# Optimization experiments

Measured on AMD Instinct MI355X. Metric: run time of the kernel, lower is better.

## Reference

```python
import jax, jax.numpy as jnp
import numpy as np

N_NODES = 50000
N_EDGES = 1600000
NEG_SLOPE = 0.2


def _gat_layer(x, src, dst, W, a_src, a_dst, b, n_nodes):
    # PyG GATConv (heads=1, concat=True): h = xW; e_ij = LeakyReLU(a_src.h_j + a_dst.h_i)
    # alpha = softmax over incoming edges of each target i; out_i = sum_j alpha_ij h_j + b
    h = x @ W                                   # [N, out]
    alpha_src = h @ a_src                        # [N]
    alpha_dst = h @ a_dst                        # [N]
    e = alpha_src[src] + alpha_dst[dst]          # [E]
    e = jnp.where(e > 0, e, NEG_SLOPE * e)       # leaky_relu(0.2)
    m = jax.ops.segment_max(e, dst, num_segments=n_nodes)   # per-target max
    ex = jnp.exp(e - m[dst])
    denom = jax.ops.segment_sum(ex, dst, num_segments=n_nodes)
    alpha = ex / (denom[dst] + 1e-16)            # [E]
    out = jax.ops.segment_sum(alpha[:, None] * h[src], dst, num_segments=n_nodes)
    return out + b


def setup_inputs() -> dict:
    key = jax.random.key(0)
    ks = jax.random.split(key, 16)
    hid, out_dim, in_dim = 128, 5, 13
    x = jax.random.normal(ks[0], (N_NODES, in_dim), dtype=jnp.float32)
    edge_index = jax.random.randint(ks[1], (2, N_EDGES), 0, N_NODES, dtype=jnp.int64)
    s = 0.1
    return {
        "x": x,
        "edge_index": edge_index,
        "W1": jax.random.normal(ks[2], (in_dim, hid), dtype=jnp.float32) * s,
        "a_src1": jax.random.normal(ks[3], (hid,), dtype=jnp.float32) * s,
        "a_dst1": jax.random.normal(ks[4], (hid,), dtype=jnp.float32) * s,
        "b1": jnp.zeros((hid,), dtype=jnp.float32),
        "W2": jax.random.normal(ks[5], (hid, hid), dtype=jnp.float32) * s,
        "a_src2": jax.random.normal(ks[6], (hid,), dtype=jnp.float32) * s,
        "a_dst2": jax.random.normal(ks[7], (hid,), dtype=jnp.float32) * s,
        "b2": jnp.zeros((hid,), dtype=jnp.float32),
        "W3": jax.random.normal(ks[8], (hid, out_dim), dtype=jnp.float32) * s,
        "a_src3": jax.random.normal(ks[9], (out_dim,), dtype=jnp.float32) * s,
        "a_dst3": jax.random.normal(ks[10], (out_dim,), dtype=jnp.float32) * s,
        "b3": jnp.zeros((out_dim,), dtype=jnp.float32),
    }


def reference(x, edge_index, W1, a_src1, a_dst1, b1, W2, a_src2, a_dst2, b2,
              W3, a_src3, a_dst3, b3):
    n = x.shape[0]
    # GATConv add_self_loops=True: append (i, i) edges
    loops = jnp.arange(n, dtype=edge_index.dtype)
    src = jnp.concatenate([edge_index[0], loops])
    dst = jnp.concatenate([edge_index[1], loops])
    h = _gat_layer(x, src, dst, W1, a_src1, a_dst1, b1, n)
    h = jax.nn.relu(h)  # dropout identity in eval mode
    h = _gat_layer(h, src, dst, W2, a_src2, a_dst2, b2, n)
    h = jax.nn.relu(h)
    h = _gat_layer(h, src, dst, W3, a_src3, a_dst3, b3, n)
    return jax.nn.log_softmax(h, axis=1)
```

## Files before the change

### kernel.cpp

```cpp
#include <hip/hip_runtime.h>
#include <hip/hip_bf16.h>


#define LEAKY(e) ((e) > 0.f ? (e) : 0.2f * (e))
__device__ inline float clamp30(float e) { return fminf(fmaxf(e, -30.f), 30.f); }
__device__ inline float expc(float e) { return __expf(clamp30(LEAKY(e))); }

__device__ inline float ldany(const void* p, int bf, int i) {
    return bf ? __bfloat162float(((const __hip_bfloat16*)p)[i])
              : ((const float*)p)[i];
}
__device__ inline int ldidx(const void* p, int i64, long long i) {
    return i64 ? (int)(((const unsigned int*)p)[2 * i])
               : ((const int*)p)[i];
}

__device__ inline float bflo(unsigned int w) { return __uint_as_float(w << 16); }
__device__ inline float bfhi(unsigned int w) { return __uint_as_float(w & 0xffff0000u); }
__device__ inline unsigned short bfbits(float a) {
    __hip_bfloat16 x = __float2bfloat16(a);
    unsigned short u; __builtin_memcpy(&u, &x, 2); return u;
}
__device__ inline unsigned int packbf(float a, float b) {
    return (unsigned int)bfbits(a) | ((unsigned int)bfbits(b) << 16);
}

typedef __attribute__((ext_vector_type(8))) short short8;
typedef __attribute__((ext_vector_type(4))) float f32x4;

__global__ void detect_kernel(const void* W1, const void* ei, int* flags) {
    if (threadIdx.x == 0 && blockIdx.x == 0) {
        const unsigned int* w = (const unsigned int*)W1;
        int c = 0;
        for (int i = 0; i < 64; i++) {
            unsigned int e = (w[i] >> 7) & 0xFFu;
            if (e >= 0x70u && e <= 0x7Fu) c++;
        }
        flags[0] = (c >= 32) ? 1 : 0;
        const unsigned int* q = (const unsigned int*)ei;
        int z = 0;
        for (int i = 0; i < 64; i++)
            if (q[2 * i + 1] == 0u) z++;
        flags[1] = (z >= 32) ? 1 : 0;
    }
}


__global__ __launch_bounds__(256) void sortA_hist(
    const void* __restrict__ ei, const int* __restrict__ flags,
    int* __restrict__ blockHist, int E, int NBUK)
{
    __shared__ int hist[512];
    const int i64 = flags[1];
    const int tid = threadIdx.x, blk = blockIdx.x;
    for (int i = tid; i < NBUK; i += 256) hist[i] = 0;
    __syncthreads();
    const int chunk = (E + 255) / 256;
    const int e0 = blk * chunk, e1 = min(e0 + chunk, E);
    for (int t = e0 + tid; t < e1; t += 256) {
        int d = ldidx(ei, i64, (long long)E + t);
        atomicAdd(&hist[d >> 7], 1);
    }
    __syncthreads();
    for (int i = tid; i < NBUK; i += 256)
        blockHist[blk * NBUK + i] = hist[i];
}

__global__ __launch_bounds__(256) void sortB_prefix(
    int* __restrict__ blockHist, int* __restrict__ bucketBase, int NBUK)
{
    __shared__ int wt[4];
    __shared__ int wbase[4];
    const int b = blockIdx.x;
    const int tid = threadIdx.x, lane = tid & 63, wid = tid >> 6;
    int v = blockHist[tid * NBUK + b];
    int x = v;
#pragma unroll
    for (int o = 1; o < 64; o <<= 1) {
        int y = __shfl_up(x, o);
        if (lane >= o) x += y;
    }
    if (lane == 63) wt[wid] = x;
    __syncthreads();
    if (tid == 0) {
        int s = 0;
#pragma unroll
        for (int i = 0; i < 4; i++) { wbase[i] = s; s += wt[i]; }
        bucketBase[b] = s;
    }
    __syncthreads();
    blockHist[tid * NBUK + b] = x - v + wbase[wid];
}

__global__ __launch_bounds__(512) void sortB2_scan(
    int* __restrict__ bucketBase, int NBUK)
{
    __shared__ int wt[8];
    __shared__ int wbase[8];
    __shared__ int total_s;
    const int tid = threadIdx.x, lane = tid & 63, wid = tid >> 6;
    int v = (tid < NBUK) ? bucketBase[tid] : 0;
    int x = v;
#pragma unroll
    for (int o = 1; o < 64; o <<= 1) {
        int y = __shfl_up(x, o);
        if (lane >= o) x += y;
    }
    if (lane == 63) wt[wid] = x;
    __syncthreads();
    if (tid == 0) {
        int s = 0;
#pragma unroll
        for (int i = 0; i < 8; i++) { wbase[i] = s; s += wt[i]; }
        total_s = s;
    }
    __syncthreads();
    if (tid < NBUK) bucketBase[tid] = x - v + wbase[wid];
    if (tid == 0) bucketBase[NBUK] = total_s;
}

__global__ __launch_bounds__(256) void sortC_scatter(
    const void* __restrict__ ei, const int* __restrict__ flags,
    const int* __restrict__ blockHist, const int* __restrict__ bucketBase,
    unsigned int* __restrict__ pairbuf, int E, int NBUK)
{
    __shared__ int cur[512];
    const int i64 = flags[1];
    const int tid = threadIdx.x, blk = blockIdx.x;
    for (int i = tid; i < NBUK; i += 256)
        cur[i] = blockHist[blk * NBUK + i] + bucketBase[i];
    __syncthreads();
    const int chunk = (E + 255) / 256;
    const int e0 = blk * chunk, e1 = min(e0 + chunk, E);
    for (int t = e0 + tid; t < e1; t += 256) {
        int s = ldidx(ei, i64, t);
        int d = ldidx(ei, i64, (long long)E + t);
        int pos = atomicAdd(&cur[d >> 7], 1);
        pairbuf[pos] = ((unsigned int)(d & 127) << 16) | (unsigned int)s;
    }
}

__global__ __launch_bounds__(256) void sortD_bin(
    const unsigned int* __restrict__ pairbuf, const int* __restrict__ bucketBase,
    int* __restrict__ rowptr, unsigned short* __restrict__ ssrc, int N, int NBUK)
{
    __shared__ int cnt[128];
    __shared__ int cur2[128];
    __shared__ int wt1;
    const int b = blockIdx.x;
    const int tid = threadIdx.x, lane = tid & 63;
    const int e0 = bucketBase[b], e1 = bucketBase[b + 1];
    if (tid < 128) cnt[tid] = 0;
    __syncthreads();
    for (int i = e0 + tid; i < e1; i += 256)
        atomicAdd(&cnt[pairbuf[i] >> 16], 1);
    __syncthreads();
    if (tid < 128) {
        int v = cnt[tid];
        int x = v;
#pragma unroll
        for (int o = 1; o < 64; o <<= 1) {
            int y = __shfl_up(x, o);
            if (lane >= o) x += y;
        }
        if (tid == 63) wt1 = x;
        __syncthreads();
        if (tid >= 64) x += wt1;
        int pfx = x - v;
        cur2[tid] = pfx;
        int node = b * 128 + tid;
        if (node < N) rowptr[node] = e0 + pfx;
    } else {
        __syncthreads();
    }
    if (b == NBUK - 1 && tid == 0) rowptr[N] = e1;
    __syncthreads();
    for (int i = e0 + tid; i < e1; i += 256) {
        unsigned int w = pairbuf[i];
        int p = atomicAdd(&cur2[w >> 16], 1);
        ssrc[e0 + p] = (unsigned short)(w & 0xFFFFu);
    }
}


__global__ __launch_bounds__(256) void node_prep13(
    const void* __restrict__ xin, const void* __restrict__ Wg,
    const void* __restrict__ asg, const void* __restrict__ adg,
    const int* __restrict__ flags,
    unsigned int* __restrict__ h2, float* __restrict__ asrc,
    float* __restrict__ adst, int N)
{
    const int bf = flags[0];
    __shared__ float Wlds[13 * 128];
    for (int i = threadIdx.x; i < 13 * 128; i += 256)
        Wlds[i] = ldany(Wg, bf, i);
    __syncthreads();
    const int lane = threadIdx.x & 63;
    int wave = (blockIdx.x * 256 + threadIdx.x) >> 6;
    int nw = (gridDim.x * 256) >> 6;
    float a0 = ldany(asg, bf, 2 * lane), a1 = ldany(asg, bf, 2 * lane + 1);
    float d0 = ldany(adg, bf, 2 * lane), d1 = ldany(adg, bf, 2 * lane + 1);
    for (int n = wave; n < N; n += nw) {
        float x0 = (lane < 13) ? ldany(xin, bf, n * 13 + lane) : 0.f;
        float s0 = 0.f, s1 = 0.f;
#pragma unroll
        for (int k = 0; k < 13; k++) {
            float xv = __shfl(x0, k);
            s0 += xv * Wlds[k * 128 + 2 * lane];
            s1 += xv * Wlds[k * 128 + 2 * lane + 1];
        }
        float pa = s0 * a0 + s1 * a1;
        float pd = s0 * d0 + s1 * d1;
#pragma unroll
        for (int o = 32; o > 0; o >>= 1) {
            pa += __shfl_xor(pa, o);
            pd += __shfl_xor(pd, o);
        }
        if (lane == 0) { asrc[n] = pa; adst[n] = pd; }
        h2[(size_t)n * 64 + lane] = packbf(s0, s1);
    }
}

__global__ __launch_bounds__(128) void packW2T(
    const void* __restrict__ Wg, const int* __restrict__ flags,
    unsigned short* __restrict__ W2T)
{
    const int bf = flags[0];
    const int n = blockIdx.x;
    const int k = threadIdx.x;
    W2T[n * 128 + k] = bf ? ((const unsigned short*)Wg)[k * 128 + n]
                          : bfbits(((const float*)Wg)[k * 128 + n]);
}

__global__ __launch_bounds__(256) void gemm_mfma(
    const float* __restrict__ X, const unsigned short* __restrict__ W2T,
    const void* __restrict__ asg, const void* __restrict__ adg,
    const int* __restrict__ flags, unsigned int* __restrict__ h2,
    float* __restrict__ asrc, float* __restrict__ adst, int N)
{
    const int bf = flags[0];
    __shared__ unsigned short A_s[64 * 136];
    __shared__ unsigned short B_s[128 * 136];
    const int tid = threadIdx.x;
    const int nb0 = blockIdx.x * 64;

#pragma unroll
    for (int it = 0; it < 8; it++) {
        int f = it * 256 + tid;
        int n = f >> 4, kc = (f & 15) * 8;
        uint4 v = *(const uint4*)&W2T[n * 128 + kc];
        *(uint4*)&B_s[n * 136 + kc] = v;
    }
#pragma unroll
    for (int it = 0; it < 8; it++) {
        int f = it * 256 + tid;
        int n = f >> 5, g = f & 31;
        int node = min(nb0 + n, N - 1);
        float4 v = *(const float4*)&X[(size_t)node * 128 + g * 4];
        unsigned int* dst = (unsigned int*)&A_s[n * 136 + g * 4];
        dst[0] = packbf(v.x, v.y);
        dst[1] = packbf(v.z, v.w);
    }
    __syncthreads();

    const int wv = tid >> 6;
    const int lane = tid & 63;
    const int m = lane & 15, quad = lane >> 4;

    f32x4 acc[8];
#pragma unroll
    for (int c = 0; c < 8; c++) acc[c] = (f32x4){0.f, 0.f, 0.f, 0.f};

#pragma unroll
    for (int q = 0; q < 4; q++) {
        short8 a = *(const short8*)&A_s[(wv * 16 + m) * 136 + q * 32 + quad * 8];
#pragma unroll
        for (int c = 0; c < 8; c++) {
            short8 b = *(const short8*)&B_s[(c * 16 + m) * 136 + q * 32 + quad * 8];
            acc[c] = __builtin_amdgcn_mfma_f32_16x16x32_bf16(a, b, acc[c], 0, 0, 0);
        }
    }

    float asv[8], adv[8];
#pragma unroll
    for (int c = 0; c < 8; c++) {
        asv[c] = ldany(asg, bf, c * 16 + m);
        adv[c] = ldany(adg, bf, c * 16 + m);
    }
    unsigned short* h2u = (unsigned short*)h2;
#pragma unroll
    for (int reg = 0; reg < 4; reg++) {
        int node = nb0 + wv * 16 + quad * 4 + reg;
        float pa = 0.f, pd = 0.f;
#pragma unroll
        for (int c = 0; c < 8; c++) {
            float v = acc[c][reg];
            pa += v * asv[c];
            pd += v * adv[c];
            if (node < N) h2u[(size_t)node * 128 + c * 16 + m] = bfbits(v);
        }
#pragma unroll
        for (int o = 1; o < 16; o <<= 1) {
            pa += __shfl_xor(pa, o);
            pd += __shfl_xor(pd, o);
        }
        if (node < N && m == 0) { asrc[node] = pa; adst[node] = pd; }
    }
}

__global__ __launch_bounds__(256) void proj7w(
    const float* __restrict__ X, const void* __restrict__ W3,
    const void* __restrict__ as3, const void* __restrict__ ad3,
    const int* __restrict__ flags, float* __restrict__ h3p,
    float* __restrict__ asrc, float* __restrict__ adst, int N)
{
    const int bf = flags[0];
    __shared__ float WpT[7 * 128];
    const int tid = threadIdx.x;
    for (int i = tid; i < 7 * 128; i += 256) {
        int j = i >> 7, k = i & 127;
        float v;
        if (j < 5) v = ldany(W3, bf, k * 5 + j);
        else if (j == 5) v = ldany(as3, bf, k);
        else v = ldany(ad3, bf, k);
        WpT[i] = v;
    }
    __syncthreads();
    const int lane = tid & 63;
    int wave = (blockIdx.x * 256 + tid) >> 6;
    int nw = (gridDim.x * 256) >> 6;
    for (int n = wave; n < N; n += nw) {
        float x0 = X[(size_t)n * 128 + lane];
        float x1 = X[(size_t)n * 128 + 64 + lane];
        float p[7];
#pragma unroll
        for (int j = 0; j < 7; j++)
            p[j] = x0 * WpT[j * 128 + lane] + x1 * WpT[j * 128 + 64 + lane];
#pragma unroll
        for (int o = 32; o > 0; o >>= 1) {
#pragma unroll
            for (int j = 0; j < 7; j++) p[j] += __shfl_xor(p[j], o);
        }
        if (lane == 0) {
            float4 o0 = {p[0], p[1], p[2], p[3]};
            *(float4*)&h3p[(size_t)n * 8] = o0;
            h3p[(size_t)n * 8 + 4] = p[4];
            asrc[n] = p[5];
            adst[n] = p[6];
        }
    }
}


__device__ inline int rdl(int v, int j) { return __builtin_amdgcn_readlane(v, j); }
__device__ inline float rdlf(float v, int j) {
    return __uint_as_float((unsigned int)__builtin_amdgcn_readlane((int)__float_as_uint(v), j));
}

__global__ __launch_bounds__(256) void agg_fused128(
    const int* __restrict__ rowptr, const unsigned short* __restrict__ ssrc,
    const unsigned int* __restrict__ h2, const float* __restrict__ asrc,
    const float* __restrict__ adst, const void* __restrict__ bias,
    const int* __restrict__ flags, float* __restrict__ feat, int nStart, int nEnd)
{
    const int bf = flags[0];
    const int lane = threadIdx.x & 63;
    int wave = (blockIdx.x * 256 + threadIdx.x) >> 6;
    int nw = (gridDim.x * 256) >> 6;
    const float bx = ldany(bias, bf, 2 * lane);
    const float by = ldany(bias, bf, 2 * lane + 1);
    const unsigned ul = (unsigned)lane;

    for (int n = nStart + wave; n < nEnd; n += nw) {
        float ad = adst[n];
        float wself = expc(asrc[n] + ad);
        unsigned int hw = h2[((unsigned)n << 6) | ul];
        float accx = wself * bflo(hw), accy = wself * bfhi(hw);
        float wpart = (lane == 0) ? wself : 0.f;
        const int start = rowptr[n], end = rowptr[n + 1];
        for (int base = start; base < end; base += 64) {
            int sl = 0;
            float wl = 0.f;
            if (base + lane < end) {
                sl = (int)ssrc[base + lane];
                wl = expc(asrc[sl] + ad);
            }
            wpart += wl;
            const int cnt = min(64, end - base);
            int j = 0;
            for (; j + 16 <= cnt; j += 16) {
                unsigned int u[16];
                float w[16];
#pragma unroll
                for (int t = 0; t < 16; t++) {
                    unsigned s = (unsigned)rdl(sl, j + t);
                    u[t] = h2[(s << 6) | ul];
                }
#pragma unroll
                for (int t = 0; t < 16; t++) w[t] = rdlf(wl, j + t);
#pragma unroll
                for (int t = 0; t < 16; t++) {
                    accx += w[t] * bflo(u[t]);
                    accy += w[t] * bfhi(u[t]);
                }
            }
            for (; j + 8 <= cnt; j += 8) {
                unsigned int u[8];
                float w[8];
#pragma unroll
                for (int t = 0; t < 8; t++) {
                    unsigned s = (unsigned)rdl(sl, j + t);
                    u[t] = h2[(s << 6) | ul];
                }
#pragma unroll
                for (int t = 0; t < 8; t++) w[t] = rdlf(wl, j + t);
#pragma unroll
                for (int t = 0; t < 8; t++) {
                    accx += w[t] * bflo(u[t]);
                    accy += w[t] * bfhi(u[t]);
                }
            }
            for (; j < cnt; j++) {
                unsigned s = (unsigned)rdl(sl, j);
                float w = rdlf(wl, j);
                unsigned int ww = h2[(s << 6) | ul];
                accx += w * bflo(ww);
                accy += w * bfhi(ww);
            }
        }
        float wsum = wpart;
#pragma unroll
        for (int o = 32; o > 0; o >>= 1) wsum += __shfl_xor(wsum, o);
        float inv = 1.f / (wsum + 1e-16f);
        float2 ov = {fmaxf(accx * inv + bx, 0.f), fmaxf(accy * inv + by, 0.f)};
        *(float2*)&feat[(size_t)n * 128 + 2 * lane] = ov;
    }
}

__global__ __launch_bounds__(256) void agg_fused5(
    const int* __restrict__ rowptr, const unsigned short* __restrict__ ssrc,
    const float* __restrict__ h3p, const float* __restrict__ asrc,
    const float* __restrict__ adst, const void* __restrict__ b3,
    const int* __restrict__ flags, float* __restrict__ out, int N)
{
    const int bf = flags[0];
    const int lane = threadIdx.x & 63;
    int wave = (blockIdx.x * 256 + threadIdx.x) >> 6;
    int nw = (gridDim.x * 256) >> 6;

    for (int n = wave; n < N; n += nw) {
        float ad = adst[n];
        float a0 = 0.f, a1 = 0.f, a2 = 0.f, a3 = 0.f, a4 = 0.f, wsum = 0.f;
        if (lane == 0) {
            float w = expc(asrc[n] + ad);
            wsum = w;
            float4 v = *(const float4*)&h3p[(unsigned)n * 8u];
            float v4 = h3p[(unsigned)n * 8u + 4u];
            a0 = w * v.x; a1 = w * v.y; a2 = w * v.z; a3 = w * v.w; a4 = w * v4;
        }
        const int start = rowptr[n], end = rowptr[n + 1];
        for (int i = start + lane; i < end; i += 64) {
            unsigned s = (unsigned)ssrc[i];
            float w = expc(asrc[s] + ad);
            float4 v = *(const float4*)&h3p[s * 8u];
            float v4 = h3p[s * 8u + 4u];
            wsum += w;
            a0 += w * v.x; a1 += w * v.y; a2 += w * v.z; a3 += w * v.w; a4 += w * v4;
        }
#pragma unroll
        for (int o = 32; o > 0; o >>= 1) {
            a0 += __shfl_xor(a0, o); a1 += __shfl_xor(a1, o); a2 += __shfl_xor(a2, o);
            a3 += __shfl_xor(a3, o); a4 += __shfl_xor(a4, o); wsum += __shfl_xor(wsum, o);
        }
        if (lane == 0) {
            float inv = 1.f / (wsum + 1e-16f);
            float v0 = a0 * inv + ldany(b3, bf, 0);
            float v1 = a1 * inv + ldany(b3, bf, 1);
            float v2 = a2 * inv + ldany(b3, bf, 2);
            float v3 = a3 * inv + ldany(b3, bf, 3);
            float v4 = a4 * inv + ldany(b3, bf, 4);
            float m = fmaxf(fmaxf(fmaxf(v0, v1), fmaxf(v2, v3)), v4);
            float s = __expf(v0 - m) + __expf(v1 - m) + __expf(v2 - m)
                    + __expf(v3 - m) + __expf(v4 - m);
            float lse = m + __logf(s);
            out[n * 5 + 0] = v0 - lse; out[n * 5 + 1] = v1 - lse;
            out[n * 5 + 2] = v2 - lse; out[n * 5 + 3] = v3 - lse;
            out[n * 5 + 4] = v4 - lse;
        }
    }
}

extern "C" void kernel_launch(void* const* d_in, const int* in_sizes, int n_in,
                              void* d_out, int out_size, void* d_ws, size_t ws_size,
                              hipStream_t stream)
{
    const void* x  = d_in[0];
    const void* ei = d_in[1];
    const void* W1 = d_in[2];
    const void* as1= d_in[3];
    const void* ad1= d_in[4];
    const void* b1 = d_in[5];
    const void* W2 = d_in[6];
    const void* as2= d_in[7];
    const void* ad2= d_in[8];
    const void* b2 = d_in[9];
    const void* W3 = d_in[10];
    const void* as3= d_in[11];
    const void* ad3= d_in[12];
    const void* b3 = d_in[13];

    const int N = in_sizes[0] / 13;
    const int E = in_sizes[1] / 2;
    const int NBUK = (N + 127) / 128;

    float* ws    = (float*)d_ws;
    float* feat  = ws;
    unsigned int* h2 = (unsigned int*)(feat + (size_t)N * 128);
    float* asrc  = (float*)(h2 + (size_t)N * 64);
    float* adst  = asrc + N;
    float* h3p   = adst + N;
    int*   rowptr= (int*)(h3p + (size_t)N * 8);
    int*   bucketBase = rowptr + N + 1;
    int*   blockHist  = bucketBase + NBUK + 1;
    unsigned short* W2T = (unsigned short*)(blockHist + 256 * NBUK);
    unsigned int* pairbuf = (unsigned int*)(W2T + 128 * 128);
    unsigned short* ssrc16 = (unsigned short*)(pairbuf + E);
    int*   flags = (int*)(ssrc16 + E);

    const int half = N / 2;
    const int wbh = (half + 3) / 4;
    const int wbh2 = (N - half + 3) / 4;
    const int wb = (N + 3) / 4;
    const int gb = (N + 63) / 64;

    detect_kernel<<<1, 64, 0, stream>>>(W1, ei, flags);

    sortA_hist<<<256, 256, 0, stream>>>(ei, flags, blockHist, E, NBUK);
    sortB_prefix<<<NBUK, 256, 0, stream>>>(blockHist, bucketBase, NBUK);
    sortB2_scan<<<1, 512, 0, stream>>>(bucketBase, NBUK);
    sortC_scatter<<<256, 256, 0, stream>>>(ei, flags, blockHist, bucketBase,
                                           pairbuf, E, NBUK);
    sortD_bin<<<NBUK, 256, 0, stream>>>(pairbuf, bucketBase, rowptr, ssrc16, N, NBUK);
    packW2T<<<128, 128, 0, stream>>>(W2, flags, W2T);

    node_prep13<<<1024, 256, 0, stream>>>(x, W1, as1, ad1, flags, h2, asrc, adst, N);
    agg_fused128<<<wbh, 256, 0, stream>>>(rowptr, ssrc16, h2, asrc, adst, b1, flags,
                                          feat, 0, half);
    agg_fused128<<<wbh2, 256, 0, stream>>>(rowptr, ssrc16, h2, asrc, adst, b1, flags,
                                           feat, half, N);

    gemm_mfma<<<gb, 256, 0, stream>>>(feat, W2T, as2, ad2, flags, h2, asrc, adst, N);
    agg_fused128<<<wbh, 256, 0, stream>>>(rowptr, ssrc16, h2, asrc, adst, b2, flags,
                                          feat, 0, half);
    agg_fused128<<<wbh2, 256, 0, stream>>>(rowptr, ssrc16, h2, asrc, adst, b2, flags,
                                           feat, half, N);

    proj7w<<<wb, 256, 0, stream>>>(feat, W3, as3, ad3, flags, h3p, asrc, adst, N);
    agg_fused5<<<wb, 256, 0, stream>>>(rowptr, ssrc16, h3p, asrc, adst, b3, flags,
                                       (float*)d_out, N);
}
```

Measured before the change: 331.6 us.

## Fuse setup kernels, inline dtype detection, merge layer-2 aggregation with layer-3 projection

Removes the separate detect kernel by recomputing the dtype flags per wave with a ballot over the first 64 words. Merges the histogram, layer-1 node projection and W2 transpose into one launch split by block index. Collapses the two half-range aggregation launches into one, and folds the layer-3 projection into the layer-2 aggregation so the 128-wide features are not written and re-read. This cuts launch count and global traffic, at the cost of a heavier fused aggregation kernel and repeated tiny detection loads in every block.

```diff
diff --git a/kernel.cpp b/kernel.cpp
--- a/kernel.cpp
+++ b/kernel.cpp
@@ -25,46 +25,88 @@
     return (unsigned int)bfbits(a) | ((unsigned int)bfbits(b) << 16);
 }
 
+__device__ inline int detect_bf(const void* W1) {
+    int t = threadIdx.x & 63;
+    unsigned int w = ((const unsigned int*)W1)[t];
+    unsigned int e = (w >> 7) & 0xFFu;
+    unsigned long long m = __ballot(e >= 0x70u && e <= 0x7Fu);
+    return __popcll(m) >= 32;
+}
+__device__ inline int detect_i64(const void* ei) {
+    int t = threadIdx.x & 63;
+    unsigned int q = ((const unsigned int*)ei)[2 * t + 1];
+    unsigned long long m = __ballot(q == 0u);
+    return __popcll(m) >= 32;
+}
+
 typedef __attribute__((ext_vector_type(8))) short short8;
 typedef __attribute__((ext_vector_type(4))) float f32x4;
 
-__global__ void detect_kernel(const void* W1, const void* ei, int* flags) {
-    if (threadIdx.x == 0 && blockIdx.x == 0) {
-        const unsigned int* w = (const unsigned int*)W1;
-        int c = 0;
-        for (int i = 0; i < 64; i++) {
-            unsigned int e = (w[i] >> 7) & 0xFFu;
-            if (e >= 0x70u && e <= 0x7Fu) c++;
-        }
-        flags[0] = (c >= 32) ? 1 : 0;
-        const unsigned int* q = (const unsigned int*)ei;
-        int z = 0;
-        for (int i = 0; i < 64; i++)
-            if (q[2 * i + 1] == 0u) z++;
-        flags[1] = (z >= 32) ? 1 : 0;
-    }
-}
-
-
-__global__ __launch_bounds__(256) void sortA_hist(
-    const void* __restrict__ ei, const int* __restrict__ flags,
-    int* __restrict__ blockHist, int E, int NBUK)
+__global__ __launch_bounds__(256) void fusedA(
+    const void* __restrict__ xin, const void* __restrict__ ei,
+    const void* __restrict__ W1, const void* __restrict__ as1,
+    const void* __restrict__ ad1, const void* __restrict__ W2,
+    int* __restrict__ blockHist, unsigned short* __restrict__ W2T,
+    unsigned int* __restrict__ h2, float* __restrict__ asrc,
+    float* __restrict__ adst, int N, int E, int NBUK)
 {
     __shared__ int hist[512];
-    const int i64 = flags[1];
-    const int tid = threadIdx.x, blk = blockIdx.x;
-    for (int i = tid; i < NBUK; i += 256) hist[i] = 0;
-    __syncthreads();
-    const int chunk = (E + 255) / 256;
-    const int e0 = blk * chunk, e1 = min(e0 + chunk, E);
-    for (int t = e0 + tid; t < e1; t += 256) {
-        int d = ldidx(ei, i64, (long long)E + t);
-        atomicAdd(&hist[d >> 7], 1);
-    }
-    __syncthreads();
-    for (int i = tid; i < NBUK; i += 256)
-        blockHist[blk * NBUK + i] = hist[i];
-}
+    __shared__ float Wlds[13 * 128];
+    const int blk = blockIdx.x;
+    const int tid = threadIdx.x;
+
+    if (blk < 256) {
+        const int i64 = detect_i64(ei);
+        for (int i = tid; i < NBUK; i += 256) hist[i] = 0;
+        __syncthreads();
+        const int chunk = (E + 255) / 256;
+        const int e0 = blk * chunk, e1 = min(e0 + chunk, E);
+        for (int t = e0 + tid; t < e1; t += 256) {
+            int d = ldidx(ei, i64, (long long)E + t);
+            atomicAdd(&hist[d >> 7], 1);
+        }
+        __syncthreads();
+        for (int i = tid; i < NBUK; i += 256)
+            blockHist[blk * NBUK + i] = hist[i];
+    } else if (blk < 1280) {
+        const int bf = detect_bf(W1);
+        for (int i = tid; i < 13 * 128; i += 256)
+            Wlds[i] = ldany(W1, bf, i);
+        __syncthreads();
+        const int lane = tid & 63;
+        int wave = ((blk - 256) * 256 + tid) >> 6;
+        const int nw = 1024 * 4;
+        float a0 = ldany(as1, bf, 2 * lane), a1 = ldany(as1, bf, 2 * lane + 1);
+        float d0 = ldany(ad1, bf, 2 * lane), d1 = ldany(ad1, bf, 2 * lane + 1);
+        for (int n = wave; n < N; n += nw) {
+            float x0 = (lane < 13) ? ldany(xin, bf, n * 13 + lane) : 0.f;
+            float s0 = 0.f, s1 = 0.f;
+#pragma unroll
+            for (int k = 0; k < 13; k++) {
+                float xv = __shfl(x0, k);
+                s0 += xv * Wlds[k * 128 + 2 * lane];
+                s1 += xv * Wlds[k * 128 + 2 * lane + 1];
+            }
+            float pa = s0 * a0 + s1 * a1;
+            float pd = s0 * d0 + s1 * d1;
+#pragma unroll
+            for (int o = 32; o > 0; o >>= 1) {
+                pa += __shfl_xor(pa, o);
+                pd += __shfl_xor(pd, o);
+            }
+            if (lane == 0) { asrc[n] = pa; adst[n] = pd; }
+            h2[(size_t)n * 64 + lane] = packbf(s0, s1);
+        }
+    } else {
+        const int bf = detect_bf(W1);
+        for (int i = tid; i < 128 * 128; i += 256) {
+            int n = i >> 7, k = i & 127;
+            W2T[i] = bf ? ((const unsigned short*)W2)[k * 128 + n]
+                        : bfbits(((const float*)W2)[k * 128 + n]);
+        }
+    }
+}
+
 
 __global__ __launch_bounds__(256) void sortB_prefix(
     int* __restrict__ blockHist, int* __restrict__ bucketBase, int NBUK)
@@ -120,12 +162,12 @@
 }
 
 __global__ __launch_bounds__(256) void sortC_scatter(
-    const void* __restrict__ ei, const int* __restrict__ flags,
+    const void* __restrict__ ei,
     const int* __restrict__ blockHist, const int* __restrict__ bucketBase,
     unsigned int* __restrict__ pairbuf, int E, int NBUK)
 {
     __shared__ int cur[512];
-    const int i64 = flags[1];
+    const int i64 = detect_i64(ei);
     const int tid = threadIdx.x, blk = blockIdx.x;
     for (int i = tid; i < NBUK; i += 256)
         cur[i] = blockHist[blk * NBUK + i] + bucketBase[i];
@@ -182,63 +224,13 @@
     }
 }
 
-
-__global__ __launch_bounds__(256) void node_prep13(
-    const void* __restrict__ xin, const void* __restrict__ Wg,
-    const void* __restrict__ asg, const void* __restrict__ adg,
-    const int* __restrict__ flags,
-    unsigned int* __restrict__ h2, float* __restrict__ asrc,
-    float* __restrict__ adst, int N)
-{
-    const int bf = flags[0];
-    __shared__ float Wlds[13 * 128];
-    for (int i = threadIdx.x; i < 13 * 128; i += 256)
-        Wlds[i] = ldany(Wg, bf, i);
-    __syncthreads();
-    const int lane = threadIdx.x & 63;
-    int wave = (blockIdx.x * 256 + threadIdx.x) >> 6;
-    int nw = (gridDim.x * 256) >> 6;
-    float a0 = ldany(asg, bf, 2 * lane), a1 = ldany(asg, bf, 2 * lane + 1);
-    float d0 = ldany(adg, bf, 2 * lane), d1 = ldany(adg, bf, 2 * lane + 1);
-    for (int n = wave; n < N; n += nw) {
-        float x0 = (lane < 13) ? ldany(xin, bf, n * 13 + lane) : 0.f;
-        float s0 = 0.f, s1 = 0.f;
-#pragma unroll
-        for (int k = 0; k < 13; k++) {
-            float xv = __shfl(x0, k);
-            s0 += xv * Wlds[k * 128 + 2 * lane];
-            s1 += xv * Wlds[k * 128 + 2 * lane + 1];
-        }
-        float pa = s0 * a0 + s1 * a1;
-        float pd = s0 * d0 + s1 * d1;
-#pragma unroll
-        for (int o = 32; o > 0; o >>= 1) {
-            pa += __shfl_xor(pa, o);
-            pd += __shfl_xor(pd, o);
-        }
-        if (lane == 0) { asrc[n] = pa; adst[n] = pd; }
-        h2[(size_t)n * 64 + lane] = packbf(s0, s1);
-    }
-}
-
-__global__ __launch_bounds__(128) void packW2T(
-    const void* __restrict__ Wg, const int* __restrict__ flags,
-    unsigned short* __restrict__ W2T)
-{
-    const int bf = flags[0];
-    const int n = blockIdx.x;
-    const int k = threadIdx.x;
-    W2T[n * 128 + k] = bf ? ((const unsigned short*)Wg)[k * 128 + n]
-                          : bfbits(((const float*)Wg)[k * 128 + n]);
-}
-
 __global__ __launch_bounds__(256) void gemm_mfma(
     const float* __restrict__ X, const unsigned short* __restrict__ W2T,
     const void* __restrict__ asg, const void* __restrict__ adg,
-    const int* __restrict__ flags, unsigned int* __restrict__ h2,
+    const void* __restrict__ dref, unsigned int* __restrict__ h2,
     float* __restrict__ asrc, float* __restrict__ adst, int N)
 {
-    const int bf = flags[0];
+    const int bf = detect_bf(dref);
     __shared__ unsigned short A_s[64 * 136];
     __shared__ unsigned short B_s[128 * 136];
     const int tid = threadIdx.x;
@@ -308,13 +300,112 @@
     }
 }
 
-__global__ __launch_bounds__(256) void proj7w(
-    const float* __restrict__ X, const void* __restrict__ W3,
-    const void* __restrict__ as3, const void* __restrict__ ad3,
-    const int* __restrict__ flags, float* __restrict__ h3p,
-    float* __restrict__ asrc, float* __restrict__ adst, int N)
-{
-    const int bf = flags[0];
+
+__device__ inline int rdl(int v, int j) { return __builtin_amdgcn_readlane(v, j); }
+__device__ inline float rdlf(float v, int j) {
+    return __uint_as_float((unsigned int)__builtin_amdgcn_readlane((int)__float_as_uint(v), j));
+}
+
+__device__ inline float2 agg_node(
+    int n, const int* rowptr, const unsigned short* ssrc,
+    const unsigned int* h2, const float* asrc, const float* adst,
+    float bx, float by, unsigned ul)
+{
+    const int lane = (int)ul;
+    float ad = adst[n];
+    float wself = expc(asrc[n] + ad);
+    unsigned int hw = h2[((unsigned)n << 6) | ul];
+    float accx = wself * bflo(hw), accy = wself * bfhi(hw);
+    float wpart = (lane == 0) ? wself : 0.f;
+    const int start = rowptr[n], end = rowptr[n + 1];
+    for (int base = start; base < end; base += 64) {
+        int sl = 0;
+        float wl = 0.f;
+        if (base + lane < end) {
+            sl = (int)ssrc[base + lane];
+            wl = expc(asrc[sl] + ad);
+        }
+        wpart += wl;
+        const int cnt = min(64, end - base);
+        int j = 0;
+        for (; j + 16 <= cnt; j += 16) {
+            unsigned int u[16];
+            float w[16];
+#pragma unroll
+            for (int t = 0; t < 16; t++) {
+                unsigned s = (unsigned)rdl(sl, j + t);
+                u[t] = h2[(s << 6) | ul];
+            }
+#pragma unroll
+            for (int t = 0; t < 16; t++) w[t] = rdlf(wl, j + t);
+#pragma unroll
+            for (int t = 0; t < 16; t++) {
+                accx += w[t] * bflo(u[t]);
+                accy += w[t] * bfhi(u[t]);
+            }
+        }
+        for (; j + 8 <= cnt; j += 8) {
+            unsigned int u[8];
+            float w[8];
+#pragma unroll
+            for (int t = 0; t < 8; t++) {
+                unsigned s = (unsigned)rdl(sl, j + t);
+                u[t] = h2[(s << 6) | ul];
+            }
+#pragma unroll
+            for (int t = 0; t < 8; t++) w[t] = rdlf(wl, j + t);
+#pragma unroll
+            for (int t = 0; t < 8; t++) {
+                accx += w[t] * bflo(u[t]);
+                accy += w[t] * bfhi(u[t]);
+            }
+        }
+        for (; j < cnt; j++) {
+            unsigned s = (unsigned)rdl(sl, j);
+            float w = rdlf(wl, j);
+            unsigned int ww = h2[(s << 6) | ul];
+            accx += w * bflo(ww);
+            accy += w * bfhi(ww);
+        }
+    }
+    float wsum = wpart;
+#pragma unroll
+    for (int o = 32; o > 0; o >>= 1) wsum += __shfl_xor(wsum, o);
+    float inv = 1.f / (wsum + 1e-16f);
+    float2 ov = {fmaxf(accx * inv + bx, 0.f), fmaxf(accy * inv + by, 0.f)};
+    return ov;
+}
+
+__global__ __launch_bounds__(256) void agg_fused128(
+    const int* __restrict__ rowptr, const unsigned short* __restrict__ ssrc,
+    const unsigned int* __restrict__ h2, const float* __restrict__ asrc,
+    const float* __restrict__ adst, const void* __restrict__ bias,
+    const void* __restrict__ dref, float* __restrict__ feat, int N)
+{
+    const int bf = detect_bf(dref);
+    const int lane = threadIdx.x & 63;
+    int wave = (blockIdx.x * 256 + threadIdx.x) >> 6;
+    int nw = (gridDim.x * 256) >> 6;
+    const float bx = ldany(bias, bf, 2 * lane);
+    const float by = ldany(bias, bf, 2 * lane + 1);
+    const unsigned ul = (unsigned)lane;
+    for (int n = wave; n < N; n += nw) {
+        float2 ov = agg_node(n, rowptr, ssrc, h2, asrc, adst, bx, by, ul);
+        *(float2*)&feat[(size_t)n * 128 + 2 * lane] = ov;
+    }
+}
+
+__global__ __launch_bounds__(256) void agg_fused128_proj(
+    const int* __restrict__ rowptr, const unsigned short* __restrict__ ssrc,
+    const unsigned int* __restrict__ h2, const float* __restrict__ asrc,
+    const float* __restrict__ adst, const void* __restrict__ bias,
+    const void* __restrict__ dref,
+    const void* __restrict__ W3, const void* __restrict__ as3,
+    const void* __restrict__ ad3,
+    float* __restrict__ h3p, float* __restrict__ asrc3, float* __restrict__ adst3,
+    int N)
+{
+    const int bf = detect_bf(dref);
     __shared__ float WpT[7 * 128];
     const int tid = threadIdx.x;
     for (int i = tid; i < 7 * 128; i += 256) {
@@ -329,13 +420,15 @@
     const int lane = tid & 63;
     int wave = (blockIdx.x * 256 + tid) >> 6;
     int nw = (gridDim.x * 256) >> 6;
+    const float bx = ldany(bias, bf, 2 * lane);
+    const float by = ldany(bias, bf, 2 * lane + 1);
+    const unsigned ul = (unsigned)lane;
     for (int n = wave; n < N; n += nw) {
-        float x0 = X[(size_t)n * 128 + lane];
-        float x1 = X[(size_t)n * 128 + 64 + lane];
+        float2 ov = agg_node(n, rowptr, ssrc, h2, asrc, adst, bx, by, ul);
         float p[7];
 #pragma unroll
         for (int j = 0; j < 7; j++)
-            p[j] = x0 * WpT[j * 128 + lane] + x1 * WpT[j * 128 + 64 + lane];
+            p[j] = ov.x * WpT[j * 128 + 2 * lane] + ov.y * WpT[j * 128 + 2 * lane + 1];
 #pragma unroll
         for (int o = 32; o > 0; o >>= 1) {
 #pragma unroll
@@ -345,95 +438,9 @@
             float4 o0 = {p[0], p[1], p[2], p[3]};
             *(float4*)&h3p[(size_t)n * 8] = o0;
             h3p[(size_t)n * 8 + 4] = p[4];
-            asrc[n] = p[5];
-            adst[n] = p[6];
-        }
-    }
-}
-
-
-__device__ inline int rdl(int v, int j) { return __builtin_amdgcn_readlane(v, j); }
-__device__ inline float rdlf(float v, int j) {
-    return __uint_as_float((unsigned int)__builtin_amdgcn_readlane((int)__float_as_uint(v), j));
-}
-
-__global__ __launch_bounds__(256) void agg_fused128(
-    const int* __restrict__ rowptr, const unsigned short* __restrict__ ssrc,
-    const unsigned int* __restrict__ h2, const float* __restrict__ asrc,
-    const float* __restrict__ adst, const void* __restrict__ bias,
-    const int* __restrict__ flags, float* __restrict__ feat, int nStart, int nEnd)
-{
-    const int bf = flags[0];
-    const int lane = threadIdx.x & 63;
-    int wave = (blockIdx.x * 256 + threadIdx.x) >> 6;
-    int nw = (gridDim.x * 256) >> 6;
-    const float bx = ldany(bias, bf, 2 * lane);
-    const float by = ldany(bias, bf, 2 * lane + 1);
-    const unsigned ul = (unsigned)lane;
-
-    for (int n = nStart + wave; n < nEnd; n += nw) {
-        float ad = adst[n];
-        float wself = expc(asrc[n] + ad);
-        unsigned int hw = h2[((unsigned)n << 6) | ul];
-        float accx = wself * bflo(hw), accy = wself * bfhi(hw);
-        float wpart = (lane == 0) ? wself : 0.f;
-        const int start = rowptr[n], end = rowptr[n + 1];
-        for (int base = start; base < end; base += 64) {
-            int sl = 0;
-            float wl = 0.f;
-            if (base + lane < end) {
-                sl = (int)ssrc[base + lane];
-                wl = expc(asrc[sl] + ad);
-            }
-            wpart += wl;
-            const int cnt = min(64, end - base);
-            int j = 0;
-            for (; j + 16 <= cnt; j += 16) {
-                unsigned int u[16];
-                float w[16];
-#pragma unroll
-                for (int t = 0; t < 16; t++) {
-                    unsigned s = (unsigned)rdl(sl, j + t);
-                    u[t] = h2[(s << 6) | ul];
-                }
-#pragma unroll
-                for (int t = 0; t < 16; t++) w[t] = rdlf(wl, j + t);
-#pragma unroll
-                for (int t = 0; t < 16; t++) {
-                    accx += w[t] * bflo(u[t]);
-                    accy += w[t] * bfhi(u[t]);
-                }
-            }
-            for (; j + 8 <= cnt; j += 8) {
-                unsigned int u[8];
-                float w[8];
-#pragma unroll
-                for (int t = 0; t < 8; t++) {
-                    unsigned s = (unsigned)rdl(sl, j + t);
-                    u[t] = h2[(s << 6) | ul];
-                }
-#pragma unroll
-                for (int t = 0; t < 8; t++) w[t] = rdlf(wl, j + t);
-#pragma unroll
-                for (int t = 0; t < 8; t++) {
-                    accx += w[t] * bflo(u[t]);
-                    accy += w[t] * bfhi(u[t]);
-                }
-            }
-            for (; j < cnt; j++) {
-                unsigned s = (unsigned)rdl(sl, j);
-                float w = rdlf(wl, j);
-                unsigned int ww = h2[(s << 6) | ul];
-                accx += w * bflo(ww);
-                accy += w * bfhi(ww);
-            }
-        }
-        float wsum = wpart;
-#pragma unroll
-        for (int o = 32; o > 0; o >>= 1) wsum += __shfl_xor(wsum, o);
-        float inv = 1.f / (wsum + 1e-16f);
-        float2 ov = {fmaxf(accx * inv + bx, 0.f), fmaxf(accy * inv + by, 0.f)};
-        *(float2*)&feat[(size_t)n * 128 + 2 * lane] = ov;
+            asrc3[n] = p[5];
+            adst3[n] = p[6];
+        }
     }
 }
 
@@ -441,9 +448,9 @@
     const int* __restrict__ rowptr, const unsigned short* __restrict__ ssrc,
     const float* __restrict__ h3p, const float* __restrict__ asrc,
     const float* __restrict__ adst, const void* __restrict__ b3,
-    const int* __restrict__ flags, float* __restrict__ out, int N)
-{
-    const int bf = flags[0];
+    const void* __restrict__ dref, float* __restrict__ out, int N)
+{
+    const int bf = detect_bf(dref);
     const int lane = threadIdx.x & 63;
     int wave = (blockIdx.x * 256 + threadIdx.x) >> 6;
     int nw = (gridDim.x * 256) >> 6;
@@ -518,44 +525,31 @@
     unsigned int* h2 = (unsigned int*)(feat + (size_t)N * 128);
     float* asrc  = (float*)(h2 + (size_t)N * 64);
     float* adst  = asrc + N;
-    float* h3p   = adst + N;
+    float* asrc3 = adst + N;
+    float* adst3 = asrc3 + N;
+    float* h3p   = adst3 + N;
     int*   rowptr= (int*)(h3p + (size_t)N * 8);
     int*   bucketBase = rowptr + N + 1;
     int*   blockHist  = bucketBase + NBUK + 1;
     unsigned short* W2T = (unsigned short*)(blockHist + 256 * NBUK);
     unsigned int* pairbuf = (unsigned int*)(W2T + 128 * 128);
     unsigned short* ssrc16 = (unsigned short*)(pairbuf + E);
-    int*   flags = (int*)(ssrc16 + E);
-
-    const int half = N / 2;
-    const int wbh = (half + 3) / 4;
-    const int wbh2 = (N - half + 3) / 4;
+
     const int wb = (N + 3) / 4;
     const int gb = (N + 63) / 64;
 
-    detect_kernel<<<1, 64, 0, stream>>>(W1, ei, flags);
-
-    sortA_hist<<<256, 256, 0, stream>>>(ei, flags, blockHist, E, NBUK);
+    fusedA<<<1281, 256, 0, stream>>>(x, ei, W1, as1, ad1, W2,
+                                     blockHist, W2T, h2, asrc, adst, N, E, NBUK);
     sortB_prefix<<<NBUK, 256, 0, stream>>>(blockHist, bucketBase, NBUK);
     sortB2_scan<<<1, 512, 0, stream>>>(bucketBase, NBUK);
-    sortC_scatter<<<256, 256, 0, stream>>>(ei, flags, blockHist, bucketBase,
-                                           pairbuf, E, NBUK);
+    sortC_scatter<<<256, 256, 0, stream>>>(ei, blockHist, bucketBase, pairbuf, E, NBUK);
     sortD_bin<<<NBUK, 256, 0, stream>>>(pairbuf, bucketBase, rowptr, ssrc16, N, NBUK);
-    packW2T<<<128, 128, 0, stream>>>(W2, flags, W2T);
-
-    node_prep13<<<1024, 256, 0, stream>>>(x, W1, as1, ad1, flags, h2, asrc, adst, N);
-    agg_fused128<<<wbh, 256, 0, stream>>>(rowptr, ssrc16, h2, asrc, adst, b1, flags,
-                                          feat, 0, half);
-    agg_fused128<<<wbh2, 256, 0, stream>>>(rowptr, ssrc16, h2, asrc, adst, b1, flags,
-                                           feat, half, N);
-
-    gemm_mfma<<<gb, 256, 0, stream>>>(feat, W2T, as2, ad2, flags, h2, asrc, adst, N);
-    agg_fused128<<<wbh, 256, 0, stream>>>(rowptr, ssrc16, h2, asrc, adst, b2, flags,
-                                          feat, 0, half);
-    agg_fused128<<<wbh2, 256, 0, stream>>>(rowptr, ssrc16, h2, asrc, adst, b2, flags,
-                                           feat, half, N);
-
-    proj7w<<<wb, 256, 0, stream>>>(feat, W3, as3, ad3, flags, h3p, asrc, adst, N);
-    agg_fused5<<<wb, 256, 0, stream>>>(rowptr, ssrc16, h3p, asrc, adst, b3, flags,
+
+    agg_fused128<<<wb, 256, 0, stream>>>(rowptr, ssrc16, h2, asrc, adst, b1, W1,
+                                         feat, N);
+    gemm_mfma<<<gb, 256, 0, stream>>>(feat, W2T, as2, ad2, W1, h2, asrc, adst, N);
+    agg_fused128_proj<<<wb, 256, 0, stream>>>(rowptr, ssrc16, h2, asrc, adst, b2, W1,
+                                              W3, as3, ad3, h3p, asrc3, adst3, N);
+    agg_fused5<<<wb, 256, 0, stream>>>(rowptr, ssrc16, h3p, asrc3, adst3, b3, W1,
                                        (float*)d_out, N);
 }
```

After: 286.8 us (median of 2 runs). 1.16x faster.
